# Performance work log

Measured on AMD Instinct MI355X. Metric: run time of the kernel, lower is better.

## Reference

```python
import jax, jax.numpy as jnp
import numpy as np

H = 1024


def setup_inputs() -> dict:
    key = jax.random.key(0)
    ks = jax.random.split(key, 7)
    x = jax.random.normal(ks[0], (8, 2048, H), dtype=jnp.float32)
    s = 1.0 / np.sqrt(H)
    Wq = jax.random.normal(ks[1], (H, H), dtype=jnp.float32) * s
    bq = jnp.zeros((H,), dtype=jnp.float32)
    Wk = jax.random.normal(ks[2], (H, H), dtype=jnp.float32) * s
    bk = jnp.zeros((H,), dtype=jnp.float32)
    Wv = jax.random.normal(ks[3], (H, H), dtype=jnp.float32) * s
    bv = jnp.zeros((H,), dtype=jnp.float32)
    return {"x": x, "Wq": Wq, "bq": bq, "Wk": Wk, "bk": bk, "Wv": Wv, "bv": bv}


def reference(x, Wq, bq, Wk, bk, Wv, bv):
    # q,k,v: [B,S,H]
    q = jnp.einsum('bsh,hd->bsd', x, Wq) + bq
    k = jnp.einsum('bsh,hd->bsd', x, Wk) + bk
    v = jnp.einsum('bsh,hd->bsd', x, Wv) + bv
    scale = 1.0 / jnp.sqrt(jnp.asarray(x.shape[-1], dtype=x.dtype))
    scores = jnp.einsum('bqd,bkd->bqk', q, k) * scale  # [B,S,S]
    attn = jax.nn.softmax(scores, axis=-1)
    return jnp.einsum('bqk,bkd->bqd', attn, v)
```

## Files before the change

kernel.cpp:

```cpp
#include <hip/hip_runtime.h>

typedef _Float16 half8  __attribute__((ext_vector_type(8)));
typedef _Float16 half4v __attribute__((ext_vector_type(4)));
typedef float    floatx4 __attribute__((ext_vector_type(4)));

#define GLD_LDS16(g, l)                                                        \
  __builtin_amdgcn_global_load_lds(                                            \
      (const __attribute__((address_space(1))) void*)(g),                      \
      (__attribute__((address_space(3))) void*)(l), 16, 0, 0)

template <int EPI>
__global__ __launch_bounds__(256) void gemm_bt(
    const _Float16* __restrict__ A, const _Float16* __restrict__ B,
    void* __restrict__ Cv, void* __restrict__ Cv2, int lda, int ldb, int ldc,
    int kdim, long long sAz, long long sBz, long long sCz,
    const float* __restrict__ b0, const float* __restrict__ b1,
    const float* __restrict__ b2, float scale) {
  __shared__ _Float16 sA[128 * 64];
  __shared__ _Float16 sB[128 * 64];

  const int z = blockIdx.z;
  A += (size_t)z * sAz;
  B += (size_t)z * sBz;

  const int tid = threadIdx.x;
  const int wid = tid >> 6;
  const int lane = tid & 63;
  const int m0 = blockIdx.y * 128;
  const int n0 = blockIdx.x * 128;

  const int wm = (wid & 1) * 64;
  const int wn = (wid >> 1) * 64;
  const int lr = lane & 15;
  const int lk = lane >> 4;

  floatx4 acc[4][4];
#pragma unroll
  for (int i = 0; i < 4; ++i)
#pragma unroll
    for (int j = 0; j < 4; ++j)
#pragma unroll
      for (int r = 0; r < 4; ++r) acc[i][j][r] = 0.f;

  for (int k0 = 0; k0 < kdim; k0 += 64) {
#pragma unroll
    for (int j = 0; j < 4; ++j) {
      const int s = j * 256 + wid * 64 + lane;
      const int ub = (j * 256 + wid * 64) * 8;
      const int row = s >> 3;
      const int kc = (s & 7) ^ (row & 7);
      GLD_LDS16(A + (size_t)(m0 + row) * lda + k0 + kc * 8, &sA[ub]);
      GLD_LDS16(B + (size_t)(n0 + row) * ldb + k0 + kc * 8, &sB[ub]);
    }
    __syncthreads();

#pragma unroll
    for (int ks = 0; ks < 2; ++ks) {
      half8 af[4], bf[4];
#pragma unroll
      for (int t = 0; t < 4; ++t) {
        const int ra = wm + t * 16 + lr;
        const int kcl = ks * 4 + lk;
        af[t] = *(const half8*)&sA[(ra * 8 + (kcl ^ (ra & 7))) * 8];
        const int rb = wn + t * 16 + lr;
        bf[t] = *(const half8*)&sB[(rb * 8 + (kcl ^ (rb & 7))) * 8];
      }
#pragma unroll
      for (int mt = 0; mt < 4; ++mt)
#pragma unroll
        for (int nt = 0; nt < 4; ++nt)
          acc[mt][nt] = __builtin_amdgcn_mfma_f32_16x16x32_f16(
              af[mt], bf[nt], acc[mt][nt], 0, 0, 0);
    }
    __syncthreads();
  }

  const float* bias = nullptr;
  if (EPI == 0) bias = (z == 0) ? b0 : ((z == 1) ? b1 : b2);

#pragma unroll
  for (int mt = 0; mt < 4; ++mt) {
#pragma unroll
    for (int nt = 0; nt < 4; ++nt) {
#pragma unroll
      for (int r = 0; r < 4; ++r) {
        const int gm = m0 + wm + mt * 16 + lk * 4 + r;
        const int gn = n0 + wn + nt * 16 + lr;
        float v = acc[mt][nt][r];
        if (EPI == 0) {
          v += bias[gn];
          if (z < 2) {
            ((_Float16*)Cv)[(size_t)z * 16777216 + (size_t)gm * 1024 + gn] =
                (_Float16)v;
          } else {
            const int b = gm >> 11, sseq = gm & 2047;
            ((_Float16*)Cv2)[(size_t)b * 2097152 + (size_t)gn * 2048 + sseq] =
                (_Float16)v;
          }
        } else if (EPI == 2) {
          ((_Float16*)Cv)[(size_t)z * sCz + (size_t)gm * ldc + gn] =
              (_Float16)(v * scale);
        } else {
          ((float*)Cv)[(size_t)z * sCz + (size_t)gm * ldc + gn] = v;
        }
      }
    }
  }
}

__global__ __launch_bounds__(256) void cvt_x(const float* __restrict__ x,
                                             _Float16* __restrict__ y) {
  const int i = blockIdx.x * 256 + threadIdx.x;
  const float4 v = ((const float4*)x)[i];
  half4v h;
  h[0] = (_Float16)v.x;
  h[1] = (_Float16)v.y;
  h[2] = (_Float16)v.z;
  h[3] = (_Float16)v.w;
  ((half4v*)y)[i] = h;
}

__global__ __launch_bounds__(256) void transpose_w(
    const float* __restrict__ W0, const float* __restrict__ W1,
    const float* __restrict__ W2, _Float16* __restrict__ Wt) {
  __shared__ float tile[32][33];
  const float* W = blockIdx.z == 0 ? W0 : (blockIdx.z == 1 ? W1 : W2);
  _Float16* T = Wt + (size_t)blockIdx.z * 1048576;
  const int d0 = blockIdx.x * 32, h0 = blockIdx.y * 32;
  const int tx = threadIdx.x, ty = threadIdx.y;
#pragma unroll
  for (int i = 0; i < 4; ++i)
    tile[ty + i * 8][tx] = W[(size_t)(h0 + ty + i * 8) * 1024 + d0 + tx];
  __syncthreads();
#pragma unroll
  for (int i = 0; i < 4; ++i)
    T[(size_t)(d0 + ty + i * 8) * 1024 + h0 + tx] =
        (_Float16)tile[tx][ty + i * 8];
}

__global__ __launch_bounds__(256) void softmax_rows(_Float16* __restrict__ S) {
  __shared__ float red[8];
  _Float16* p = S + (size_t)blockIdx.x * 2048;
  const int tid = threadIdx.x;
  const int wid = tid >> 6, lane = tid & 63;

  half8 hv = *(const half8*)&p[tid * 8];
  float f[8];
#pragma unroll
  for (int i = 0; i < 8; ++i) f[i] = (float)hv[i];

  float m = f[0];
#pragma unroll
  for (int i = 1; i < 8; ++i) m = fmaxf(m, f[i]);
#pragma unroll
  for (int o = 32; o > 0; o >>= 1) m = fmaxf(m, __shfl_xor(m, o));
  if (lane == 0) red[wid] = m;
  __syncthreads();
  m = fmaxf(fmaxf(red[0], red[1]), fmaxf(red[2], red[3]));

  float s = 0.f;
#pragma unroll
  for (int i = 0; i < 8; ++i) {
    f[i] = exp2f((f[i] - m) * 1.44269504088896f);
    s += f[i];
  }
#pragma unroll
  for (int o = 32; o > 0; o >>= 1) s += __shfl_xor(s, o);
  if (lane == 0) red[4 + wid] = s;
  __syncthreads();
  s = red[4] + red[5] + red[6] + red[7];
  const float inv = 1.f / s;

  half8 out;
#pragma unroll
  for (int i = 0; i < 8; ++i) out[i] = (_Float16)(f[i] * inv);
  *(half8*)&p[tid * 8] = out;
}

extern "C" void kernel_launch(void* const* d_in, const int* in_sizes, int n_in,
                              void* d_out, int out_size, void* d_ws,
                              size_t ws_size, hipStream_t stream) {
  const float* x = (const float*)d_in[0];
  const float* Wq = (const float*)d_in[1];
  const float* bq = (const float*)d_in[2];
  const float* Wk = (const float*)d_in[3];
  const float* bk = (const float*)d_in[4];
  const float* Wv = (const float*)d_in[5];
  const float* bv = (const float*)d_in[6];
  float* out = (float*)d_out;

  char* w = (char*)d_ws;
  _Float16* xb = (_Float16*)(w);
  _Float16* Wt = (_Float16*)(w + 33554432);
  _Float16* QK = (_Float16*)(w + 39845888);
  _Float16* Vt = (_Float16*)(w + 106954752);
  _Float16* S  = (_Float16*)(w + 140509184);

  cvt_x<<<16384, 256, 0, stream>>>(x, xb);
  transpose_w<<<dim3(32, 32, 3), dim3(32, 8), 0, stream>>>(Wq, Wk, Wv, Wt);
  gemm_bt<0><<<dim3(8, 128, 3), 256, 0, stream>>>(
      xb, Wt, QK, Vt, 1024, 1024, 1024, 1024, 0LL, 1048576LL, 0LL, bq, bk, bv,
      1.f);
  gemm_bt<2><<<dim3(16, 16, 8), 256, 0, stream>>>(
      QK, QK + 16777216, S, nullptr, 1024, 1024, 2048, 1024, 2097152LL,
      2097152LL, 4194304LL, nullptr, nullptr, nullptr, 0.03125f);
  softmax_rows<<<16384, 256, 0, stream>>>(S);
  gemm_bt<3><<<dim3(8, 16, 8), 256, 0, stream>>>(
      S, Vt, out, nullptr, 2048, 2048, 1024, 2048, 4194304LL, 2097152LL,
      2097152LL, nullptr, nullptr, nullptr, 1.f);

  (void)in_sizes;
  (void)n_in;
  (void)out_size;
  (void)ws_size;
}
```

Baseline: 488.9 us.

## Switch GEMM to 32x32x16 MFMA, hoist load pointers, merge prep kernels

```diff
diff --git a/kernel.cpp b/kernel.cpp
--- a/kernel.cpp
+++ b/kernel.cpp
@@ -1,8 +1,8 @@
 #include <hip/hip_runtime.h>
 
-typedef _Float16 half8  __attribute__((ext_vector_type(8)));
-typedef _Float16 half4v __attribute__((ext_vector_type(4)));
-typedef float    floatx4 __attribute__((ext_vector_type(4)));
+typedef _Float16 half8   __attribute__((ext_vector_type(8)));
+typedef _Float16 half4v  __attribute__((ext_vector_type(4)));
+typedef float    floatx16 __attribute__((ext_vector_type(16)));
 
 #define GLD_LDS16(g, l)                                                        \
   __builtin_amdgcn_global_load_lds(                                            \
@@ -31,45 +31,55 @@
 
   const int wm = (wid & 1) * 64;
   const int wn = (wid >> 1) * 64;
-  const int lr = lane & 15;
-  const int lk = lane >> 4;
-
-  floatx4 acc[4][4];
-#pragma unroll
-  for (int i = 0; i < 4; ++i)
-#pragma unroll
-    for (int j = 0; j < 4; ++j)
-#pragma unroll
-      for (int r = 0; r < 4; ++r) acc[i][j][r] = 0.f;
+  const int l31 = lane & 31;
+  const int khi = lane >> 5;
+
+  floatx16 acc[2][2];
+#pragma unroll
+  for (int i = 0; i < 2; ++i)
+#pragma unroll
+    for (int j = 0; j < 2; ++j)
+#pragma unroll
+      for (int r = 0; r < 16; ++r) acc[i][j][r] = 0.f;
+
+  const _Float16* gA[4];
+  const _Float16* gB[4];
+#pragma unroll
+  for (int j = 0; j < 4; ++j) {
+    const int s = j * 256 + wid * 64 + lane;
+    const int row = s >> 3;
+    const int kc = (s & 7) ^ (row & 7);
+    gA[j] = A + (size_t)(m0 + row) * lda + kc * 8;
+    gB[j] = B + (size_t)(n0 + row) * ldb + kc * 8;
+  }
 
   for (int k0 = 0; k0 < kdim; k0 += 64) {
 #pragma unroll
     for (int j = 0; j < 4; ++j) {
-      const int s = j * 256 + wid * 64 + lane;
       const int ub = (j * 256 + wid * 64) * 8;
-      const int row = s >> 3;
-      const int kc = (s & 7) ^ (row & 7);
-      GLD_LDS16(A + (size_t)(m0 + row) * lda + k0 + kc * 8, &sA[ub]);
-      GLD_LDS16(B + (size_t)(n0 + row) * ldb + k0 + kc * 8, &sB[ub]);
+      GLD_LDS16(gA[j], &sA[ub]);
+      GLD_LDS16(gB[j], &sB[ub]);
+      gA[j] += 64;
+      gB[j] += 64;
     }
     __syncthreads();
 
 #pragma unroll
-    for (int ks = 0; ks < 2; ++ks) {
-      half8 af[4], bf[4];
-#pragma unroll
-      for (int t = 0; t < 4; ++t) {
-        const int ra = wm + t * 16 + lr;
-        const int kcl = ks * 4 + lk;
-        af[t] = *(const half8*)&sA[(ra * 8 + (kcl ^ (ra & 7))) * 8];
-        const int rb = wn + t * 16 + lr;
-        bf[t] = *(const half8*)&sB[(rb * 8 + (kcl ^ (rb & 7))) * 8];
+    for (int ks = 0; ks < 4; ++ks) {
+      half8 af[2], bf[2];
+      const int kc = ks * 2 + khi;
+#pragma unroll
+      for (int t = 0; t < 2; ++t) {
+        const int ra = wm + t * 32 + l31;
+        af[t] = *(const half8*)&sA[(ra * 8 + (kc ^ (ra & 7))) * 8];
+        const int rb = wn + t * 32 + l31;
+        bf[t] = *(const half8*)&sB[(rb * 8 + (kc ^ (rb & 7))) * 8];
       }
 #pragma unroll
-      for (int mt = 0; mt < 4; ++mt)
-#pragma unroll
-        for (int nt = 0; nt < 4; ++nt)
-          acc[mt][nt] = __builtin_amdgcn_mfma_f32_16x16x32_f16(
+      for (int mt = 0; mt < 2; ++mt)
+#pragma unroll
+        for (int nt = 0; nt < 2; ++nt)
+          acc[mt][nt] = __builtin_amdgcn_mfma_f32_32x32x16_f16(
               af[mt], bf[nt], acc[mt][nt], 0, 0, 0);
     }
     __syncthreads();
@@ -79,13 +89,14 @@
   if (EPI == 0) bias = (z == 0) ? b0 : ((z == 1) ? b1 : b2);
 
 #pragma unroll
-  for (int mt = 0; mt < 4; ++mt) {
-#pragma unroll
-    for (int nt = 0; nt < 4; ++nt) {
-#pragma unroll
-      for (int r = 0; r < 4; ++r) {
-        const int gm = m0 + wm + mt * 16 + lk * 4 + r;
-        const int gn = n0 + wn + nt * 16 + lr;
+  for (int mt = 0; mt < 2; ++mt) {
+#pragma unroll
+    for (int nt = 0; nt < 2; ++nt) {
+#pragma unroll
+      for (int r = 0; r < 16; ++r) {
+        const int gm =
+            m0 + wm + mt * 32 + ((r & 3) + 8 * (r >> 2) + 4 * khi);
+        const int gn = n0 + wn + nt * 32 + l31;
         float v = acc[mt][nt][r];
         if (EPI == 0) {
           v += bias[gn];
@@ -108,26 +119,31 @@
   }
 }
 
-__global__ __launch_bounds__(256) void cvt_x(const float* __restrict__ x,
-                                             _Float16* __restrict__ y) {
-  const int i = blockIdx.x * 256 + threadIdx.x;
-  const float4 v = ((const float4*)x)[i];
-  half4v h;
-  h[0] = (_Float16)v.x;
-  h[1] = (_Float16)v.y;
-  h[2] = (_Float16)v.z;
-  h[3] = (_Float16)v.w;
-  ((half4v*)y)[i] = h;
-}
-
-__global__ __launch_bounds__(256) void transpose_w(
+__global__ __launch_bounds__(256) void prep(
+    const float* __restrict__ x, _Float16* __restrict__ xb,
     const float* __restrict__ W0, const float* __restrict__ W1,
     const float* __restrict__ W2, _Float16* __restrict__ Wt) {
+  const int bid = blockIdx.x;
+  const int tid = threadIdx.x;
+  if (bid < 16384) {
+    const int i = bid * 256 + tid;
+    const float4 v = ((const float4*)x)[i];
+    half4v h;
+    h[0] = (_Float16)v.x;
+    h[1] = (_Float16)v.y;
+    h[2] = (_Float16)v.z;
+    h[3] = (_Float16)v.w;
+    ((half4v*)xb)[i] = h;
+    return;
+  }
   __shared__ float tile[32][33];
-  const float* W = blockIdx.z == 0 ? W0 : (blockIdx.z == 1 ? W1 : W2);
-  _Float16* T = Wt + (size_t)blockIdx.z * 1048576;
-  const int d0 = blockIdx.x * 32, h0 = blockIdx.y * 32;
-  const int tx = threadIdx.x, ty = threadIdx.y;
+  const int q = bid - 16384;
+  const int bz = q >> 10;
+  const int t = q & 1023;
+  const int d0 = (t & 31) * 32, h0 = (t >> 5) * 32;
+  const float* W = bz == 0 ? W0 : (bz == 1 ? W1 : W2);
+  _Float16* T = Wt + (size_t)bz * 1048576;
+  const int tx = tid & 31, ty = tid >> 5;
 #pragma unroll
   for (int i = 0; i < 4; ++i)
     tile[ty + i * 8][tx] = W[(size_t)(h0 + ty + i * 8) * 1024 + d0 + tx];
@@ -196,8 +212,7 @@
   _Float16* Vt = (_Float16*)(w + 106954752);
   _Float16* S  = (_Float16*)(w + 140509184);
 
-  cvt_x<<<16384, 256, 0, stream>>>(x, xb);
-  transpose_w<<<dim3(32, 32, 3), dim3(32, 8), 0, stream>>>(Wq, Wk, Wv, Wt);
+  prep<<<19456, 256, 0, stream>>>(x, xb, Wq, Wk, Wv, Wt);
   gemm_bt<0><<<dim3(8, 128, 3), 256, 0, stream>>>(
       xb, Wt, QK, Vt, 1024, 1024, 1024, 1024, 0LL, 1048576LL, 0LL, bq, bk, bv,
       1.f);
```

Result: no change. 493.2 us (+0.9%).

## Double-buffer GEMM LDS tiles and merge input prep kernels into one launch

Applied to the files above, without the earlier changes.

```diff
diff --git a/kernel.cpp b/kernel.cpp
--- a/kernel.cpp
+++ b/kernel.cpp
@@ -16,8 +16,8 @@
     int kdim, long long sAz, long long sBz, long long sCz,
     const float* __restrict__ b0, const float* __restrict__ b1,
     const float* __restrict__ b2, float scale) {
-  __shared__ _Float16 sA[128 * 64];
-  __shared__ _Float16 sB[128 * 64];
+  __shared__ _Float16 sA[2][128 * 64];
+  __shared__ _Float16 sB[2][128 * 64];
 
   const int z = blockIdx.z;
   A += (size_t)z * sAz;
@@ -42,36 +42,65 @@
 #pragma unroll
       for (int r = 0; r < 4; ++r) acc[i][j][r] = 0.f;
 
-  for (int k0 = 0; k0 < kdim; k0 += 64) {
-#pragma unroll
-    for (int j = 0; j < 4; ++j) {
-      const int s = j * 256 + wid * 64 + lane;
-      const int ub = (j * 256 + wid * 64) * 8;
-      const int row = s >> 3;
-      const int kc = (s & 7) ^ (row & 7);
-      GLD_LDS16(A + (size_t)(m0 + row) * lda + k0 + kc * 8, &sA[ub]);
-      GLD_LDS16(B + (size_t)(n0 + row) * ldb + k0 + kc * 8, &sB[ub]);
+  const _Float16* gA[4];
+  const _Float16* gB[4];
+  int ub[4];
+#pragma unroll
+  for (int j = 0; j < 4; ++j) {
+    const int s = j * 256 + wid * 64 + lane;
+    const int row = s >> 3;
+    const int kc = (s & 7) ^ (row & 7);
+    gA[j] = A + (size_t)(m0 + row) * lda + kc * 8;
+    gB[j] = B + (size_t)(n0 + row) * ldb + kc * 8;
+    ub[j] = (j * 256 + wid * 64) * 8;
+  }
+
+#pragma unroll
+  for (int j = 0; j < 4; ++j) {
+    GLD_LDS16(gA[j], &sA[0][ub[j]]);
+    GLD_LDS16(gB[j], &sB[0][ub[j]]);
+    gA[j] += 64;
+    gB[j] += 64;
+  }
+  __syncthreads();
+
+  const int niter = kdim >> 6;
+  for (int it = 0; it < niter; ++it) {
+    const int cur = it & 1;
+
+    half8 af[2][4], bf[2][4];
+#pragma unroll
+    for (int ks = 0; ks < 2; ++ks) {
+#pragma unroll
+      for (int t = 0; t < 4; ++t) {
+        const int kcl = ks * 4 + lk;
+        const int ra = wm + t * 16 + lr;
+        af[ks][t] = *(const half8*)&sA[cur][(ra * 8 + (kcl ^ (ra & 7))) * 8];
+        const int rb = wn + t * 16 + lr;
+        bf[ks][t] = *(const half8*)&sB[cur][(rb * 8 + (kcl ^ (rb & 7))) * 8];
+      }
     }
-    __syncthreads();
-
-#pragma unroll
-    for (int ks = 0; ks < 2; ++ks) {
-      half8 af[4], bf[4];
-#pragma unroll
-      for (int t = 0; t < 4; ++t) {
-        const int ra = wm + t * 16 + lr;
-        const int kcl = ks * 4 + lk;
-        af[t] = *(const half8*)&sA[(ra * 8 + (kcl ^ (ra & 7))) * 8];
-        const int rb = wn + t * 16 + lr;
-        bf[t] = *(const half8*)&sB[(rb * 8 + (kcl ^ (rb & 7))) * 8];
+
+    if (it + 1 < niter) {
+      const int nxt = cur ^ 1;
+#pragma unroll
+      for (int j = 0; j < 4; ++j) {
+        GLD_LDS16(gA[j], &sA[nxt][ub[j]]);
+        GLD_LDS16(gB[j], &sB[nxt][ub[j]]);
+        gA[j] += 64;
+        gB[j] += 64;
       }
+    }
+
+#pragma unroll
+    for (int ks = 0; ks < 2; ++ks)
 #pragma unroll
       for (int mt = 0; mt < 4; ++mt)
 #pragma unroll
         for (int nt = 0; nt < 4; ++nt)
           acc[mt][nt] = __builtin_amdgcn_mfma_f32_16x16x32_f16(
-              af[mt], bf[nt], acc[mt][nt], 0, 0, 0);
-    }
+              af[ks][mt], bf[ks][nt], acc[mt][nt], 0, 0, 0);
+
     __syncthreads();
   }
 
@@ -108,26 +137,31 @@
   }
 }
 
-__global__ __launch_bounds__(256) void cvt_x(const float* __restrict__ x,
-                                             _Float16* __restrict__ y) {
-  const int i = blockIdx.x * 256 + threadIdx.x;
-  const float4 v = ((const float4*)x)[i];
-  half4v h;
-  h[0] = (_Float16)v.x;
-  h[1] = (_Float16)v.y;
-  h[2] = (_Float16)v.z;
-  h[3] = (_Float16)v.w;
-  ((half4v*)y)[i] = h;
-}
-
-__global__ __launch_bounds__(256) void transpose_w(
+__global__ __launch_bounds__(256) void prep(
+    const float* __restrict__ x, _Float16* __restrict__ xb,
     const float* __restrict__ W0, const float* __restrict__ W1,
     const float* __restrict__ W2, _Float16* __restrict__ Wt) {
+  const int bid = blockIdx.x;
+  const int tid = threadIdx.x;
+  if (bid < 16384) {
+    const int i = bid * 256 + tid;
+    const float4 v = ((const float4*)x)[i];
+    half4v h;
+    h[0] = (_Float16)v.x;
+    h[1] = (_Float16)v.y;
+    h[2] = (_Float16)v.z;
+    h[3] = (_Float16)v.w;
+    ((half4v*)xb)[i] = h;
+    return;
+  }
   __shared__ float tile[32][33];
-  const float* W = blockIdx.z == 0 ? W0 : (blockIdx.z == 1 ? W1 : W2);
-  _Float16* T = Wt + (size_t)blockIdx.z * 1048576;
-  const int d0 = blockIdx.x * 32, h0 = blockIdx.y * 32;
-  const int tx = threadIdx.x, ty = threadIdx.y;
+  const int q = bid - 16384;
+  const int bz = q >> 10;
+  const int t = q & 1023;
+  const int d0 = (t & 31) * 32, h0 = (t >> 5) * 32;
+  const float* W = bz == 0 ? W0 : (bz == 1 ? W1 : W2);
+  _Float16* T = Wt + (size_t)bz * 1048576;
+  const int tx = tid & 31, ty = tid >> 5;
 #pragma unroll
   for (int i = 0; i < 4; ++i)
     tile[ty + i * 8][tx] = W[(size_t)(h0 + ty + i * 8) * 1024 + d0 + tx];
@@ -196,8 +230,7 @@
   _Float16* Vt = (_Float16*)(w + 106954752);
   _Float16* S  = (_Float16*)(w + 140509184);
 
-  cvt_x<<<16384, 256, 0, stream>>>(x, xb);
-  transpose_w<<<dim3(32, 32, 3), dim3(32, 8), 0, stream>>>(Wq, Wk, Wv, Wt);
+  prep<<<19456, 256, 0, stream>>>(x, xb, Wq, Wk, Wv, Wt);
   gemm_bt<0><<<dim3(8, 128, 3), 256, 0, stream>>>(
       xb, Wt, QK, Vt, 1024, 1024, 1024, 1024, 0LL, 1048576LL, 0LL, bq, bk, bv,
       1.f);
```

After: 480.6 us. Within noise of the previous version (-1.7%).
